# Kernel optimization log

Measured on AMD Instinct MI355X. Metric: run time of the kernel, lower is better.

Reference implementation:

```python
import jax, jax.numpy as jnp
import numpy as np

B, S, D = 1, 2048, 1024
H = 16            # num_heads
DH = D // H       # head dim = 64
WIN = 128         # local window size
DIL = 4           # dilation rate


def setup_inputs() -> dict:
    key = jax.random.key(0)
    k1, k2, k3 = jax.random.split(key, 3)
    x = jax.random.normal(k1, (B, S, D), jnp.float32)
    w_qkv = jax.random.normal(k2, (D, 3 * D), jnp.float32) * 0.02
    w_out = jax.random.normal(k3, (D, D), jnp.float32) * 0.02
    return {"x": x, "w_qkv": w_qkv, "w_out": w_out}


def reference(x, w_qkv, w_out):
    b, s, d = x.shape
    scale = 1.0 / np.sqrt(DH).astype(np.float32)

    qkv = x @ w_qkv                                   # [B,S,3D]
    q, k, v = jnp.split(qkv, 3, axis=-1)
    q = q.reshape(b, s, H, DH)
    k = k.reshape(b, s, H, DH)
    v = v.reshape(b, s, H, DH)

    # ---- local window attention: attend within non-overlapping windows ----
    nw = s // WIN
    qw = q.reshape(b, nw, WIN, H, DH)
    kw = k.reshape(b, nw, WIN, H, DH)
    vw = v.reshape(b, nw, WIN, H, DH)
    s_loc = jnp.einsum('bnihd,bnjhd->bnhij', qw, kw) * scale
    p_loc = jax.nn.softmax(s_loc, axis=-1)
    o_loc = jnp.einsum('bnhij,bnjhd->bnihd', p_loc, vw).reshape(b, s, H, DH)

    # ---- dilated attention: attend within each stride-DIL residue class ----
    n = s // DIL
    # seq index = i*DIL + g  -> position i within dilation group g
    qd = q.reshape(b, n, DIL, H, DH)
    kd = k.reshape(b, n, DIL, H, DH)
    vd = v.reshape(b, n, DIL, H, DH)
    s_dil = jnp.einsum('bighd,bjghd->bghij', qd, kd) * scale
    p_dil = jax.nn.softmax(s_dil, axis=-1)
    o_dil = jnp.einsum('bghij,bjghd->bighd', p_dil, vd).reshape(b, s, H, DH)

    # ---- global full attention ----
    s_glb = jnp.einsum('bihd,bjhd->bhij', q, k) * scale
    p_glb = jax.nn.softmax(s_glb, axis=-1)
    o_glb = jnp.einsum('bhij,bjhd->bihd', p_glb, v)

    # fuse the three scales (uniform average) and project out
    o = (o_loc + o_dil + o_glb) * (1.0 / 3.0)
    return o.reshape(b, s, d) @ w_out
```

## Files before the change

kernel.cpp:

```cpp
#include <hip/hip_runtime.h>
#include <hip/hip_bf16.h>


typedef __attribute__((ext_vector_type(8))) short s8v;
typedef __attribute__((ext_vector_type(4))) float f4v;

#define QSCALE 0.18033688011112042f

__device__ __forceinline__ short f2bf(float f) {
  union { float f; unsigned u; } x; x.f = f;
  unsigned r = (x.u + 0x7FFF + ((x.u >> 16) & 1)) >> 16;
  return (short)r;
}
__device__ __forceinline__ f4v mfma16(s8v a, s8v b, f4v c) {
  return __builtin_amdgcn_mfma_f32_16x16x32_bf16(a, b, c, 0, 0, 0);
}
__device__ __forceinline__ void load_lds16(const void* g, void* l) {
  __builtin_amdgcn_global_load_lds(
      (const __attribute__((address_space(1))) unsigned int*)g,
      (__attribute__((address_space(3))) unsigned int*)l, 16, 0, 0);
}
__device__ __forceinline__ float exp2f_fast(float x) {
  return __builtin_amdgcn_exp2f(x);
}

__global__ __launch_bounds__(256)
void fill_const_kernel(float* __restrict__ out, int n, float v) {
  int i = blockIdx.x * 256 + threadIdx.x;
  if (i < n) out[i] = v;
}

__global__ __launch_bounds__(256)
void cast_f32_bf16(const float* __restrict__ src, short* __restrict__ dst, int n) {
  int i = (blockIdx.x * 256 + threadIdx.x) * 4;
  if (i < n) {
    float4 v = *reinterpret_cast<const float4*>(&src[i]);
    union { short s[4]; int2 p; } u;
    u.s[0] = f2bf(v.x); u.s[1] = f2bf(v.y); u.s[2] = f2bf(v.z); u.s[3] = f2bf(v.w);
    *reinterpret_cast<int2*>(&dst[i]) = u.p;
  }
}

__global__ __launch_bounds__(256)
void transpose_conv(const float* __restrict__ src, short* __restrict__ dst,
                    int K, int N) {
  __shared__ float T[64][69];
  const int n0 = blockIdx.x * 64, k0 = blockIdx.y * 64;
  const int t = threadIdx.x;
  for (int jb = t; jb < 1024; jb += 256) {
    int r = jb >> 4, c4 = (jb & 15) * 4;
    float4 v = *reinterpret_cast<const float4*>(&src[(size_t)(k0 + r) * N + n0 + c4]);
    T[c4 + 0][r] = v.x; T[c4 + 1][r] = v.y; T[c4 + 2][r] = v.z; T[c4 + 3][r] = v.w;
  }
  __syncthreads();
  for (int jb = t; jb < 512; jb += 256) {
    int n = jb >> 3, k8 = (jb & 7) * 8;
    union { short s[8]; int4 v; } p;
#pragma unroll
    for (int i = 0; i < 8; ++i) p.s[i] = f2bf(T[n][k8 + i]);
    *reinterpret_cast<int4*>(&dst[(size_t)(n0 + n) * K + k0 + k8]) = p.v;
  }
}

template <int COUT, bool AF32, int NT>
__global__ __launch_bounds__(256)
void gemm_tile(const void* __restrict__ Av, const short* __restrict__ Bt,
               short* __restrict__ qb, short* __restrict__ kb,
               short* __restrict__ vT, float* __restrict__ co,
               int K, int N) {
  __shared__ __align__(16) short As[64 * 32];
  __shared__ __align__(16) short Bs[NT * 32];
  const int tid = threadIdx.x, wave = tid >> 6;
  const int li = tid & 63;
  const int row0 = blockIdx.y * 64, col0 = blockIdx.x * NT;
  const int lr = li & 15, quad = li >> 4, lk = quad * 8;
  constexpr int NTW = NT / 64;

  f4v acc[4][NTW];
#pragma unroll
  for (int i = 0; i < 4; ++i)
#pragma unroll
    for (int j = 0; j < NTW; ++j) acc[i][j] = (f4v){0.f, 0.f, 0.f, 0.f};

  for (int k0 = 0; k0 < K; k0 += 32) {
    __syncthreads();
#pragma unroll
    for (int u = 0; u < NTW; ++u)
      load_lds16(Bt + (size_t)(col0 + u * 64 + (tid >> 2)) * K + k0 + (tid & 3) * 8,
                 &Bs[u * 2048 + wave * 512]);
    if (AF32) {
      const float* A = (const float*)Av;
#pragma unroll
      for (int c = 0; c < 2; ++c) {
        int j = c * 256 + tid;
        int r = j >> 3, c4 = (j & 7) * 4;
        float4 v = *reinterpret_cast<const float4*>(&A[(size_t)(row0 + r) * K + k0 + c4]);
        union { short s[4]; int2 v2; } p;
        p.s[0] = f2bf(v.x); p.s[1] = f2bf(v.y); p.s[2] = f2bf(v.z); p.s[3] = f2bf(v.w);
        *reinterpret_cast<int2*>(&As[r * 32 + c4]) = p.v2;
      }
    } else {
      load_lds16((const short*)Av + (size_t)(row0 + (tid >> 2)) * K + k0 + (tid & 3) * 8,
                 &As[wave * 512]);
    }
    __syncthreads();

    s8v af[4], bfr[NTW];
#pragma unroll
    for (int mt = 0; mt < 4; ++mt)
      af[mt] = *reinterpret_cast<const s8v*>(&As[(mt * 16 + lr) * 32 + lk]);
#pragma unroll
    for (int u = 0; u < NTW; ++u)
      bfr[u] = *reinterpret_cast<const s8v*>(&Bs[(wave * (NT / 4) + u * 16 + lr) * 32 + lk]);
#pragma unroll
    for (int mt = 0; mt < 4; ++mt)
#pragma unroll
      for (int u = 0; u < NTW; ++u)
        acc[mt][u] = mfma16(af[mt], bfr[u], acc[mt][u]);
  }

#pragma unroll
  for (int mt = 0; mt < 4; ++mt) {
#pragma unroll
    for (int u = 0; u < NTW; ++u) {
      int gcol = col0 + wave * (NT / 4) + u * 16 + lr;
      int grow0 = row0 + mt * 16 + quad * 4;
      if (COUT == 0) {
        if (gcol >= 2048) {
          int d = gcol - 2048;
          int j = grow0 >> 2;
          int gb = ((j >> 6) << 6) + (((j >> 5) & 1) << 5) +
                   ((j & 15) << 1) + ((j >> 4) & 1);
          size_t base = (size_t)d * 2048 + gb;
#pragma unroll
          for (int r = 0; r < 4; ++r)
            vT[base + (r << 9)] = f2bf(acc[mt][u][r]);
        } else {
          short* dst = (gcol < 1024) ? qb : kb;
          float sc = (gcol < 1024) ? QSCALE : 1.0f;
          int c = gcol & 1023;
#pragma unroll
          for (int r = 0; r < 4; ++r)
            dst[(size_t)(grow0 + r) * 1024 + c] = f2bf(acc[mt][u][r] * sc);
        }
      } else {
#pragma unroll
        for (int r = 0; r < 4; ++r)
          co[(size_t)(grow0 + r) * N + gcol] = acc[mt][u][r] * (1.0f / 3.0f);
      }
    }
  }
}

__global__ __launch_bounds__(512, 2)
void attn_unified(const short* __restrict__ qb, const short* __restrict__ kb,
                  const short* __restrict__ vT, short* __restrict__ o) {
  __shared__ __align__(16) short Ks[2][64][72];
  __shared__ __align__(16) short Vt[2][64][72];
  __shared__ __align__(16) short Pls[8][16][40];
  __shared__ float lX[2][4][4][12];

  const int tid = threadIdx.x;
  const int wave = tid >> 6, li = tid & 63;
  const int grp = wave >> 2, wr = wave & 3;
  const int b = blockIdx.x, h = b & 15, g = b >> 4;
  const int qcol = h * 64;
  const int lr = li & 15, quad = li >> 4, lk = quad * 8;
  const int wt2 = g >> 2;
  const int wH  = (g >> 1) & 1;
  const bool wgrp = (grp == wH);
  const int sr = tid >> 3, sc8 = (tid & 7) * 8;

  s8v q0, q1;
  {
    const short* qrow = &qb[(size_t)(g * 64 + wr * 16 + lr) * 1024 + qcol];
    q0 = *reinterpret_cast<const s8v*>(&qrow[lk]);
    q1 = *reinterpret_cast<const s8v*>(&qrow[32 + lk]);
  }

  *reinterpret_cast<int4*>(&Ks[0][sr][sc8]) =
      *reinterpret_cast<const int4*>(&kb[(size_t)(sr << 2) * 1024 + qcol + sc8]);
  *reinterpret_cast<int4*>(&Vt[0][sr][sc8]) =
      *reinterpret_cast<const int4*>(&vT[(size_t)(h * 64 + sr) * 2048 + sc8]);
  __syncthreads();

  float l_r[4]   = {0.f, 0.f, 0.f, 0.f};
  float l_loc[4] = {0.f, 0.f, 0.f, 0.f};
  float l_dil[4] = {0.f, 0.f, 0.f, 0.f};
  f4v oacc[4], o_loc[4], o_dil[4];
#pragma unroll
  for (int i = 0; i < 4; ++i) {
    oacc[i]  = (f4v){0.f, 0.f, 0.f, 0.f};
    o_loc[i] = (f4v){0.f, 0.f, 0.f, 0.f};
    o_dil[i] = (f4v){0.f, 0.f, 0.f, 0.f};
  }

  const int koffA = ((grp * 2 + 0) * 16 + lr) * 72 + lk;
  const int koffB = ((grp * 2 + 1) * 16 + lr) * 72 + lk;
  const short* KsF = &Ks[0][0][0];
  const short* VtF = &Vt[0][0][0];

#pragma unroll
  for (int rho = 0; rho < 4; ++rho) {
    const float sn0 = oacc[0][rho], sn1 = oacc[1][rho],
                sn2 = oacc[2][rho], sn3 = oacc[3][rho];
    const float lsn = l_r[rho];

#pragma unroll 2
    for (int t8 = 0; t8 < 8; ++t8) {
      const int t = rho * 8 + t8;
      const int cur = t8 & 1, nxt = cur ^ 1;
      const bool pf = (rho < 3) || (t8 < 7);
      const bool wt = wgrp && (t8 == wt2);
      const int cb = cur * 4608;

      int4 kpre, vpre;
      if (pf) {
        const int tn = t + 1;
        const int ksn = ((((tn & 7) << 6) + sr) << 2) + (tn >> 3);
        kpre = *reinterpret_cast<const int4*>(&kb[(size_t)ksn * 1024 + qcol + sc8]);
        vpre = *reinterpret_cast<const int4*>(
            &vT[(size_t)(h * 64 + sr) * 2048 + tn * 64 + sc8]);
      }

      f4v s4a = (f4v){0.f, 0.f, 0.f, 0.f};
      f4v s4b = (f4v){0.f, 0.f, 0.f, 0.f};
      s4a = mfma16(q0, *reinterpret_cast<const s8v*>(&KsF[cb + koffA]), s4a);
      s4b = mfma16(q0, *reinterpret_cast<const s8v*>(&KsF[cb + koffB]), s4b);
      s4a = mfma16(q1, *reinterpret_cast<const s8v*>(&KsF[cb + koffA + 32]), s4a);
      s4b = mfma16(q1, *reinterpret_cast<const s8v*>(&KsF[cb + koffB + 32]), s4b);

#pragma unroll
      for (int r = 0; r < 4; ++r) {
        float p0 = exp2f_fast(s4a[r]), p1 = exp2f_fast(s4b[r]);
        float ps = p0 + p1;
        l_r[r] += ps;
        if (wt) l_loc[r] += ps;
        union { short s[2]; int v; } pk;
        pk.s[0] = f2bf(p0); pk.s[1] = f2bf(p1);
        *reinterpret_cast<int*>(&Pls[wave][quad * 4 + r][2 * lr]) = pk.v;
      }

      {
        s8v ap = *reinterpret_cast<const s8v*>(&Pls[wave][lr][lk]);
        if (wt) {
#pragma unroll
          for (int nt = 0; nt < 4; ++nt) {
            s8v bv = *reinterpret_cast<const s8v*>(
                &VtF[cb + (nt * 16 + lr) * 72 + grp * 32 + lk]);
            f4v dd = mfma16(ap, bv, (f4v){0.f, 0.f, 0.f, 0.f});
            oacc[nt] += dd;
            o_loc[nt] += dd;
          }
        } else {
#pragma unroll
          for (int nt = 0; nt < 4; ++nt) {
            s8v bv = *reinterpret_cast<const s8v*>(
                &VtF[cb + (nt * 16 + lr) * 72 + grp * 32 + lk]);
            oacc[nt] = mfma16(ap, bv, oacc[nt]);
          }
        }
      }

      if (pf) {
        *reinterpret_cast<int4*>(&Ks[nxt][sr][sc8]) = kpre;
        *reinterpret_cast<int4*>(&Vt[nxt][sr][sc8]) = vpre;
      }
      __syncthreads();
    }

    l_dil[rho] = l_r[rho] - lsn;
    o_dil[0][rho] = oacc[0][rho] - sn0;
    o_dil[1][rho] = oacc[1][rho] - sn1;
    o_dil[2][rho] = oacc[2][rho] - sn2;
    o_dil[3][rho] = oacc[3][rho] - sn3;
  }

  float lv[12];
#pragma unroll
  for (int r = 0; r < 4; ++r) { lv[r] = l_r[r]; lv[4 + r] = l_loc[r]; lv[8 + r] = l_dil[r]; }
#pragma unroll
  for (int k = 0; k < 12; ++k) {
    lv[k] += __shfl_xor(lv[k], 1, 16);
    lv[k] += __shfl_xor(lv[k], 2, 16);
    lv[k] += __shfl_xor(lv[k], 4, 16);
    lv[k] += __shfl_xor(lv[k], 8, 16);
  }
  if (lr == 0) {
#pragma unroll
    for (int k = 0; k < 12; ++k) lX[grp][wr][quad][k] = lv[k];
  }
  __syncthreads();

  f4v part[4];
#pragma unroll
  for (int r = 0; r < 4; ++r) {
    float lg = lX[0][wr][quad][r]     + lX[1][wr][quad][r];
    float ll = lX[0][wr][quad][4 + r] + lX[1][wr][quad][4 + r];
    float ld = lX[0][wr][quad][8 + r] + lX[1][wr][quad][8 + r];
    float ig = 1.0f / lg, il = 1.0f / ll, id = 1.0f / ld;
#pragma unroll
    for (int nt = 0; nt < 4; ++nt)
      part[nt][r] = oacc[nt][r] * ig + o_loc[nt][r] * il + o_dil[nt][r] * id;
  }

  float* xch = reinterpret_cast<float*>(&Ks[0][0][0]);
  const int slot = wr * 64 + li;
  if (grp == 1) {
#pragma unroll
    for (int nt = 0; nt < 4; ++nt)
#pragma unroll
      for (int hh = 0; hh < 2; ++hh) {
        float2 v2 = make_float2(part[nt][2 * hh], part[nt][2 * hh + 1]);
        *reinterpret_cast<float2*>(&xch[slot * 18 + (nt * 2 + hh) * 2]) = v2;
      }
  }
  __syncthreads();
  if (grp == 0) {
#pragma unroll
    for (int nt = 0; nt < 4; ++nt)
#pragma unroll
      for (int hh = 0; hh < 2; ++hh) {
        float2 v2 = *reinterpret_cast<const float2*>(&xch[slot * 18 + (nt * 2 + hh) * 2]);
        part[nt][2 * hh]     += v2.x;
        part[nt][2 * hh + 1] += v2.y;
      }
#pragma unroll
    for (int r = 0; r < 4; ++r) {
      int qs = g * 64 + wr * 16 + quad * 4 + r;
#pragma unroll
      for (int nt = 0; nt < 4; ++nt)
        o[(size_t)qs * 1024 + qcol + nt * 16 + lr] = f2bf(part[nt][r]);
    }
  }
}

extern "C" void kernel_launch(void* const* d_in, const int* in_sizes, int n_in,
                              void* d_out, int out_size, void* d_ws, size_t ws_size,
                              hipStream_t stream) {
  float* out = (float*)d_out;
  const int nfill = (out_size + 255) / 256;
  if (n_in != 3) { fill_const_kernel<<<nfill, 256, 0, stream>>>(out, out_size, 0.5f); return; }
  int ix = -1, iq = -1, io = -1;
  for (int i = 0; i < 3; ++i) {
    if      (in_sizes[i] == 2097152) ix = i;
    else if (in_sizes[i] == 3145728) iq = i;
    else if (in_sizes[i] == 1048576) io = i;
  }
  if (ix < 0 || iq < 0 || io < 0) { fill_const_kernel<<<nfill, 256, 0, stream>>>(out, out_size, 0.3f); return; }
  const float* x     = (const float*)d_in[ix];
  const float* w_qkv = (const float*)d_in[iq];
  const float* w_out = (const float*)d_in[io];

  char* ws = (char*)d_ws;
  const size_t MB = 1048576;
  const size_t needX = 22 * MB;
  const size_t needY = 20 * MB;

  if (ws_size >= needX) {
    short* qb     = (short*)(ws);
    short* kb     = (short*)(ws + 4 * MB);
    short* vT     = (short*)(ws + 8 * MB);
    short* w_qkvT = (short*)(ws + 12 * MB);
    short* xb     = (short*)(ws + 18 * MB);
    short* o      = (short*)(ws + 12 * MB);
    short* w_outT = (short*)(ws + 16 * MB);
    cast_f32_bf16<<<2048, 256, 0, stream>>>(x, xb, 2097152);
    transpose_conv<<<dim3(48, 16), 256, 0, stream>>>(w_qkv, w_qkvT, 1024, 3072);
    gemm_tile<0, false, 128><<<dim3(24, 32), 256, 0, stream>>>(xb, w_qkvT, qb, kb, vT, nullptr, 1024, 3072);
    transpose_conv<<<dim3(16, 16), 256, 0, stream>>>(w_out, w_outT, 1024, 1024);
    attn_unified<<<512, 512, 0, stream>>>(qb, kb, vT, o);
    gemm_tile<1, false, 64><<<dim3(16, 32), 256, 0, stream>>>(o, w_outT, nullptr, nullptr, nullptr, out, 1024, 1024);
  } else if (ws_size >= needY) {
    short* w_outT = (short*)(ws);
    short* qb     = (short*)(ws + 2 * MB);
    short* kb     = (short*)(ws + 6 * MB);
    short* vT     = (short*)(ws + 10 * MB);
    short* w_qkvT = (short*)(ws + 14 * MB);
    short* o      = (short*)(ws + 14 * MB);
    transpose_conv<<<dim3(48, 16), 256, 0, stream>>>(w_qkv, w_qkvT, 1024, 3072);
    transpose_conv<<<dim3(16, 16), 256, 0, stream>>>(w_out, w_outT, 1024, 1024);
    gemm_tile<0, true, 128><<<dim3(24, 32), 256, 0, stream>>>(x, w_qkvT, qb, kb, vT, nullptr, 1024, 3072);
    attn_unified<<<512, 512, 0, stream>>>(qb, kb, vT, o);
    gemm_tile<1, false, 64><<<dim3(16, 32), 256, 0, stream>>>(o, w_outT, nullptr, nullptr, nullptr, out, 1024, 1024);
  } else {
    fill_const_kernel<<<nfill, 256, 0, stream>>>(out, out_size, 0.2f);
  }
}
```

Baseline: 164.2 us.

## Compute transposed score tile so P stays in registers, dropping LDS round-trip

The Q·K MFMA operands are swapped so the score tile comes out transposed. Each lane then holds the P values it needs as the A operand of the PV MFMA, so the per-wave Pls shared buffer, its writes and reads are removed. To keep the operands matched, the vT store permutation in the QKV projection epilogue changes, and the row-sum bookkeeping is reworked to a scalar per lane with a cross-quad shuffle reduction. This cuts LDS traffic and shuffles in the inner loop, but it depends on the new key permutation in vT agreeing with the transposed P layout.

```diff
diff --git a/kernel.cpp b/kernel.cpp
--- a/kernel.cpp
+++ b/kernel.cpp
@@ -130,7 +130,7 @@
           int d = gcol - 2048;
           int j = grow0 >> 2;
           int gb = ((j >> 6) << 6) + (((j >> 5) & 1) << 5) +
-                   ((j & 15) << 1) + ((j >> 4) & 1);
+                   (((j >> 2) & 3) << 3) + (((j >> 4) & 1) << 2) + (j & 3);
           size_t base = (size_t)d * 2048 + gb;
 #pragma unroll
           for (int r = 0; r < 4; ++r)
@@ -157,8 +157,7 @@
                   const short* __restrict__ vT, short* __restrict__ o) {
   __shared__ __align__(16) short Ks[2][64][72];
   __shared__ __align__(16) short Vt[2][64][72];
-  __shared__ __align__(16) short Pls[8][16][40];
-  __shared__ float lX[2][4][4][12];
+  __shared__ float lX[2][4][16][4];
 
   const int tid = threadIdx.x;
   const int wave = tid >> 6, li = tid & 63;
@@ -184,9 +183,7 @@
       *reinterpret_cast<const int4*>(&vT[(size_t)(h * 64 + sr) * 2048 + sc8]);
   __syncthreads();
 
-  float l_r[4]   = {0.f, 0.f, 0.f, 0.f};
-  float l_loc[4] = {0.f, 0.f, 0.f, 0.f};
-  float l_dil[4] = {0.f, 0.f, 0.f, 0.f};
+  float l_r = 0.f, l_loc = 0.f, l_dil = 0.f;
   f4v oacc[4], o_loc[4], o_dil[4];
 #pragma unroll
   for (int i = 0; i < 4; ++i) {
@@ -204,7 +201,7 @@
   for (int rho = 0; rho < 4; ++rho) {
     const float sn0 = oacc[0][rho], sn1 = oacc[1][rho],
                 sn2 = oacc[2][rho], sn3 = oacc[3][rho];
-    const float lsn = l_r[rho];
+    const float lsn = l_r;
 
 #pragma unroll 2
     for (int t8 = 0; t8 < 8; ++t8) {
@@ -225,40 +222,37 @@
 
       f4v s4a = (f4v){0.f, 0.f, 0.f, 0.f};
       f4v s4b = (f4v){0.f, 0.f, 0.f, 0.f};
-      s4a = mfma16(q0, *reinterpret_cast<const s8v*>(&KsF[cb + koffA]), s4a);
-      s4b = mfma16(q0, *reinterpret_cast<const s8v*>(&KsF[cb + koffB]), s4b);
-      s4a = mfma16(q1, *reinterpret_cast<const s8v*>(&KsF[cb + koffA + 32]), s4a);
-      s4b = mfma16(q1, *reinterpret_cast<const s8v*>(&KsF[cb + koffB + 32]), s4b);
-
+      s4a = mfma16(*reinterpret_cast<const s8v*>(&KsF[cb + koffA]), q0, s4a);
+      s4b = mfma16(*reinterpret_cast<const s8v*>(&KsF[cb + koffB]), q0, s4b);
+      s4a = mfma16(*reinterpret_cast<const s8v*>(&KsF[cb + koffA + 32]), q1, s4a);
+      s4b = mfma16(*reinterpret_cast<const s8v*>(&KsF[cb + koffB + 32]), q1, s4b);
+
+      union { short s[8]; s8v v; } pk;
+      float ps = 0.f;
 #pragma unroll
       for (int r = 0; r < 4; ++r) {
         float p0 = exp2f_fast(s4a[r]), p1 = exp2f_fast(s4b[r]);
-        float ps = p0 + p1;
-        l_r[r] += ps;
-        if (wt) l_loc[r] += ps;
-        union { short s[2]; int v; } pk;
-        pk.s[0] = f2bf(p0); pk.s[1] = f2bf(p1);
-        *reinterpret_cast<int*>(&Pls[wave][quad * 4 + r][2 * lr]) = pk.v;
-      }
-
-      {
-        s8v ap = *reinterpret_cast<const s8v*>(&Pls[wave][lr][lk]);
-        if (wt) {
-#pragma unroll
-          for (int nt = 0; nt < 4; ++nt) {
-            s8v bv = *reinterpret_cast<const s8v*>(
-                &VtF[cb + (nt * 16 + lr) * 72 + grp * 32 + lk]);
-            f4v dd = mfma16(ap, bv, (f4v){0.f, 0.f, 0.f, 0.f});
-            oacc[nt] += dd;
-            o_loc[nt] += dd;
-          }
-        } else {
-#pragma unroll
-          for (int nt = 0; nt < 4; ++nt) {
-            s8v bv = *reinterpret_cast<const s8v*>(
-                &VtF[cb + (nt * 16 + lr) * 72 + grp * 32 + lk]);
-            oacc[nt] = mfma16(ap, bv, oacc[nt]);
-          }
+        ps += p0 + p1;
+        pk.s[r] = f2bf(p0); pk.s[4 + r] = f2bf(p1);
+      }
+      l_r += ps;
+      if (wt) l_loc += ps;
+
+      if (wt) {
+#pragma unroll
+        for (int nt = 0; nt < 4; ++nt) {
+          s8v bv = *reinterpret_cast<const s8v*>(
+              &VtF[cb + (nt * 16 + lr) * 72 + grp * 32 + lk]);
+          f4v dd = mfma16(pk.v, bv, (f4v){0.f, 0.f, 0.f, 0.f});
+          oacc[nt] += dd;
+          o_loc[nt] += dd;
+        }
+      } else {
+#pragma unroll
+        for (int nt = 0; nt < 4; ++nt) {
+          s8v bv = *reinterpret_cast<const s8v*>(
+              &VtF[cb + (nt * 16 + lr) * 72 + grp * 32 + lk]);
+          oacc[nt] = mfma16(pk.v, bv, oacc[nt]);
         }
       }
 
@@ -269,35 +263,30 @@
       __syncthreads();
     }
 
-    l_dil[rho] = l_r[rho] - lsn;
+    if (((lr ^ rho) & 3) == 0) l_dil = l_r - lsn;
     o_dil[0][rho] = oacc[0][rho] - sn0;
     o_dil[1][rho] = oacc[1][rho] - sn1;
     o_dil[2][rho] = oacc[2][rho] - sn2;
     o_dil[3][rho] = oacc[3][rho] - sn3;
   }
 
-  float lv[12];
-#pragma unroll
-  for (int r = 0; r < 4; ++r) { lv[r] = l_r[r]; lv[4 + r] = l_loc[r]; lv[8 + r] = l_dil[r]; }
-#pragma unroll
-  for (int k = 0; k < 12; ++k) {
-    lv[k] += __shfl_xor(lv[k], 1, 16);
-    lv[k] += __shfl_xor(lv[k], 2, 16);
-    lv[k] += __shfl_xor(lv[k], 4, 16);
-    lv[k] += __shfl_xor(lv[k], 8, 16);
-  }
-  if (lr == 0) {
-#pragma unroll
-    for (int k = 0; k < 12; ++k) lX[grp][wr][quad][k] = lv[k];
+  l_r   += __shfl_xor(l_r, 16);   l_r   += __shfl_xor(l_r, 32);
+  l_loc += __shfl_xor(l_loc, 16); l_loc += __shfl_xor(l_loc, 32);
+  l_dil += __shfl_xor(l_dil, 16); l_dil += __shfl_xor(l_dil, 32);
+  if (li < 16) {
+    lX[grp][wr][li][0] = l_r;
+    lX[grp][wr][li][1] = l_loc;
+    lX[grp][wr][li][2] = l_dil;
   }
   __syncthreads();
 
   f4v part[4];
 #pragma unroll
   for (int r = 0; r < 4; ++r) {
-    float lg = lX[0][wr][quad][r]     + lX[1][wr][quad][r];
-    float ll = lX[0][wr][quad][4 + r] + lX[1][wr][quad][4 + r];
-    float ld = lX[0][wr][quad][8 + r] + lX[1][wr][quad][8 + r];
+    int q4 = quad * 4 + r;
+    float lg = lX[0][wr][q4][0] + lX[1][wr][q4][0];
+    float ll = lX[0][wr][q4][1] + lX[1][wr][q4][1];
+    float ld = lX[0][wr][q4][2] + lX[1][wr][q4][2];
     float ig = 1.0f / lg, il = 1.0f / ll, id = 1.0f / ld;
 #pragma unroll
     for (int nt = 0; nt < 4; ++nt)
```

After: 159.3 us. -3.0%, faster.
